# Optimization experiments

Hardware: AMD Instinct MI355X
Metric: run time of the kernel (lower is better)

Reference implementation:

```python
import jax, jax.numpy as jnp
import numpy as np

B, T, E = 2, 2048, 1024   # batch, block_size, emb_d
H, D = 16, 64             # heads, head_size


def setup_inputs() -> dict:
    key = jax.random.key(0)
    ks = jax.random.split(key, 7)
    s = 1.0 / np.sqrt(E)
    inputs = jax.random.normal(ks[0], (B, T, E), dtype=jnp.float32)
    k_w = jax.random.uniform(ks[1], (H, E, D), jnp.float32, -s, s)
    k_b = jax.random.uniform(ks[2], (H, D), jnp.float32, -s, s)
    q_w = jax.random.uniform(ks[3], (H, E, D), jnp.float32, -s, s)
    q_b = jax.random.uniform(ks[4], (H, D), jnp.float32, -s, s)
    v_w = jax.random.uniform(ks[5], (H, E, D), jnp.float32, -s, s)
    v_b = jax.random.uniform(ks[6], (H, D), jnp.float32, -s, s)
    return {"inputs": inputs, "k_w": k_w, "k_b": k_b,
            "q_w": q_w, "q_b": q_b, "v_w": v_w, "v_b": v_b}


def reference(inputs, k_w, k_b, q_w, q_b, v_w, v_b):
    # Per-head linear projections, vectorized over heads: (B,T,E)x(H,E,D)->(B,H,T,D)
    k = jnp.einsum('bte,hed->bhtd', inputs, k_w) + k_b[None, :, None, :]
    q = jnp.einsum('bte,hed->bhtd', inputs, q_w) + q_b[None, :, None, :]
    v = jnp.einsum('bte,hed->bhtd', inputs, v_w) + v_b[None, :, None, :]

    scale = D ** (-0.5)
    # scores: (B,H,Tq,Tk)
    w = jnp.einsum('bhtd,bhsd->bhts', q, k) * scale
    tril = jnp.tril(jnp.ones((T, T), dtype=bool))
    w = jnp.where(tril[None, None, :, :], w, -jnp.inf)
    # NOTE: original torch code does softmax(weights, dim=1) on a (B,T,T)
    # tensor, i.e. over the QUERY axis. Faithfully reproduce: axis=-2 here.
    w = jax.nn.softmax(w, axis=-2)
    out = jnp.einsum('bhts,bhsd->bhtd', w, v)           # (B,H,T,D)
    # concat heads along last dim, head-major order matching torch.cat
    return out.transpose(0, 2, 1, 3).reshape(B, T, H * D)
```

## Files before the change

kernel.cpp:

```cpp
#include <hip/hip_runtime.h>
#include <hip/hip_bf16.h>
#include <math.h>

#define B_ 2
#define T_ 2048
#define E_ 1024
#define H_ 16
#define D_ 64
#define NT_ 32
#define QSCALE 0.180336880f

typedef __attribute__((ext_vector_type(8))) short bf16x8;
typedef __attribute__((ext_vector_type(4))) float f32x4;

#if __has_builtin(__builtin_amdgcn_exp2f)
#define EXP2(x) __builtin_amdgcn_exp2f(x)
#else
#define EXP2(x) exp2f(x)
#endif

__device__ __forceinline__ unsigned short f2bf(float x) {
  union { float f; unsigned u; } v; v.f = x;
  unsigned r = v.u + 0x7FFFu + ((v.u >> 16) & 1u);
  return (unsigned short)(r >> 16);
}
__device__ __forceinline__ unsigned pk2bf(float a, float b) {
  __hip_bfloat162 h = __float22bfloat162_rn(make_float2(a, b));
  union { __hip_bfloat162 h; unsigned u; } c; c.h = h; return c.u;
}

__device__ __forceinline__ void dma8(const unsigned short* g, int gstride,
                                     unsigned short* l, int lane)
{
  const int r = lane >> 3, bg = (lane & 7) ^ (r & 7);
  __builtin_amdgcn_global_load_lds(
      (const __attribute__((address_space(1))) void*)(g + (size_t)r * gstride + bg * 8),
      (__attribute__((address_space(3))) void*)l, 16, 0, 0);
}
__device__ __forceinline__ bf16x8 frag(const unsigned short* tile, int row, int g) {
  return *(const bf16x8*)(tile + row * 64 + (((g ^ row) & 7) << 3));
}

__global__ __launch_bounds__(256) void inpack_kernel(const float* __restrict__ in,
                                                     unsigned short* __restrict__ o) {
  const size_t i = ((size_t)blockIdx.x * 256 + threadIdx.x) * 8;
  float4 f0 = *(const float4*)(in + i);
  float4 f1 = *(const float4*)(in + i + 4);
  unsigned u[4] = { pk2bf(f0.x, f0.y), pk2bf(f0.z, f0.w),
                    pk2bf(f1.x, f1.y), pk2bf(f1.z, f1.w) };
  *(bf16x8*)(o + i) = *(const bf16x8*)u;
}

__global__ __launch_bounds__(256) void wpack_kernel(
    const float* __restrict__ qw, const float* __restrict__ kw, const float* __restrict__ vw,
    unsigned short* __restrict__ qwt, unsigned short* __restrict__ kwt,
    unsigned short* __restrict__ vwt)
{
  __shared__ float s[64][65];
  const int tid = threadIdx.x;
  const int e0 = blockIdx.x * 64, h = blockIdx.y, z = blockIdx.z;
  const float* w = (z == 0) ? qw : (z == 1) ? kw : vw;
  unsigned short* o = (z == 0) ? qwt : (z == 1) ? kwt : vwt;
  {
    const int r = tid >> 2;
    #pragma unroll
    for (int p = 0; p < 4; ++p) {
      const int c = (tid & 3) * 4 + p * 16;
      float4 f = *(const float4*)(w + ((size_t)(h * E_ + e0 + r)) * D_ + c);
      s[r][c] = f.x; s[r][c+1] = f.y; s[r][c+2] = f.z; s[r][c+3] = f.w;
    }
  }
  __syncthreads();
  {
    const int d = tid >> 2, ec = (tid & 3) * 16;
    unsigned short tmp[16];
    #pragma unroll
    for (int j = 0; j < 16; ++j) tmp[j] = f2bf(s[ec + j][d]);
    unsigned short* dst = o + ((size_t)(h * D_ + d)) * E_ + e0 + ec;
    *(bf16x8*)(dst)     = *(const bf16x8*)&tmp[0];
    *(bf16x8*)(dst + 8) = *(const bf16x8*)&tmp[8];
  }
}

__global__ __launch_bounds__(256) void proj_kernel(
    const unsigned short* __restrict__ in16,
    const unsigned short* __restrict__ qwt, const unsigned short* __restrict__ kwt,
    const unsigned short* __restrict__ vwt,
    const float* __restrict__ qb, const float* __restrict__ kb, const float* __restrict__ vb,
    unsigned short* __restrict__ qo, unsigned short* __restrict__ ko,
    unsigned short* __restrict__ vt)
{
  __shared__ __align__(16) unsigned short in_s[2][128 * 64];
  __shared__ __align__(16) unsigned short w_s[2][3][64 * 64];
  const int tid = threadIdx.x;
  const int lane = tid & 63, wv = tid >> 6;
  const int l15 = lane & 15, quad = lane >> 4;
  const int t0 = blockIdx.x * 128, h = blockIdx.y, b = blockIdx.z;
  const int bh = b * H_ + h;
  const unsigned short* wts[3] = { qwt, kwt, vwt };

  f32x4 acc[3][2][4];
  #pragma unroll
  for (int x = 0; x < 3; ++x)
    #pragma unroll
    for (int s = 0; s < 2; ++s)
      #pragma unroll
      for (int nb = 0; nb < 4; ++nb) acc[x][s][nb] = (f32x4){0.f, 0.f, 0.f, 0.f};

#define PROJ_STAGE(e0_, bi_)                                                      \
  {                                                                               \
    const unsigned short* gin = in16 + ((size_t)(b * T_ + t0)) * E_ + (e0_);      \
    _Pragma("unroll")                                                             \
    for (int p = 0; p < 4; ++p) {                                                 \
      const int br = wv * 32 + p * 8;                                             \
      dma8(gin + (size_t)br * E_, E_, &in_s[bi_][br * 64], lane);                 \
    }                                                                             \
    _Pragma("unroll")                                                             \
    for (int j = 0; j < 6; ++j) {                                                 \
      const int idx = wv * 6 + j;                                                 \
      const int x = idx >> 3, br = (idx & 7) * 8;                                 \
      dma8(wts[x] + ((size_t)(h * D_ + br)) * E_ + (e0_), E_,                     \
           &w_s[bi_][x][br * 64], lane);                                          \
    }                                                                             \
  }

  PROJ_STAGE(0, 0);
  __syncthreads();
  for (int e = 0; e < 16; ++e) {
    const int bi = e & 1;
    if (e < 15) PROJ_STAGE((e + 1) * 64, bi ^ 1);
    const unsigned short* is = in_s[bi];
    #pragma unroll
    for (int kk = 0; kk < 2; ++kk) {
      const int g0 = kk * 4 + quad;
      bf16x8 a0 = frag(is, wv * 32 + l15, g0);
      bf16x8 a1 = frag(is, wv * 32 + 16 + l15, g0);
      #pragma unroll
      for (int x = 0; x < 3; ++x) {
        const unsigned short* ws = w_s[bi][x];
        #pragma unroll
        for (int nb = 0; nb < 4; ++nb) {
          bf16x8 bfr = frag(ws, nb * 16 + l15, g0);
          acc[x][0][nb] = __builtin_amdgcn_mfma_f32_16x16x32_bf16(a0, bfr, acc[x][0][nb], 0, 0, 0);
          acc[x][1][nb] = __builtin_amdgcn_mfma_f32_16x16x32_bf16(a1, bfr, acc[x][1][nb], 0, 0, 0);
        }
      }
    }
    __syncthreads();
  }
#undef PROJ_STAGE

  const size_t obase = (size_t)bh * T_;
  #pragma unroll
  for (int x = 0; x < 2; ++x) {
    const float scl = (x == 0) ? QSCALE : 1.0f;
    const float* bias = (x == 0) ? qb : kb;
    unsigned short* outp = (x == 0) ? qo : ko;
    #pragma unroll
    for (int nb = 0; nb < 4; ++nb) {
      const int d = nb * 16 + l15;
      const float bvv = bias[h * D_ + d];
      #pragma unroll
      for (int s = 0; s < 2; ++s)
        #pragma unroll
        for (int r = 0; r < 4; ++r) {
          const int t = t0 + wv * 32 + s * 16 + quad * 4 + r;
          outp[(obase + t) * D_ + d] = f2bf((acc[x][s][nb][r] + bvv) * scl);
        }
    }
  }
  #pragma unroll
  for (int nb = 0; nb < 4; ++nb) {
    const int d = nb * 16 + l15;
    const float bvv = vb[h * D_ + d];
    #pragma unroll
    for (int s = 0; s < 2; ++s) {
      const int t = t0 + wv * 32 + s * 16 + quad * 4;
      unsigned short pk[4];
      #pragma unroll
      for (int r = 0; r < 4; ++r) pk[r] = f2bf(acc[2][s][nb][r] + bvv);
      *(ushort4*)(vt + ((size_t)(bh * D_ + d)) * T_ + t) = *(const ushort4*)pk;
    }
  }
}

__global__ __launch_bounds__(256) void stats_kernel(
    const unsigned short* __restrict__ q, const unsigned short* __restrict__ k,
    float* __restrict__ l)
{
  __shared__ __align__(16) unsigned short q_s[2][64 * 64];
  __shared__ float red[4][64];
  const int tid = threadIdx.x;
  const int lane = tid & 63, wv = tid >> 6;
  const int l15 = lane & 15, quad = lane >> 4;
  const int sa = blockIdx.x >> 1, p = blockIdx.x & 1;
  const int tt0 = sa + ((sa ^ p) & 1);
  if (tt0 >= NT_) return;
  const int bh = blockIdx.z * H_ + blockIdx.y;
  const int s0 = sa * 64;
  const unsigned short* qbase = q + (size_t)bh * T_ * 64;

  bf16x8 kf[4][2];
  #pragma unroll
  for (int nb = 0; nb < 4; ++nb)
    #pragma unroll
    for (int kk = 0; kk < 2; ++kk)
      kf[nb][kk] = *(const bf16x8*)(k + ((size_t)(bh * T_ + s0 + nb * 16 + l15)) * 64
                                      + kk * 32 + quad * 8);

  #pragma unroll
  for (int pp = 0; pp < 2; ++pp) {
    const int br = wv * 16 + pp * 8;
    dma8(qbase + (size_t)(tt0 * 64 + br) * 64, 64, &q_s[0][br * 64], lane);
  }
  __syncthreads();

  float lsum[4] = {0.f, 0.f, 0.f, 0.f};

  for (int tt = tt0, i = 0; tt < NT_; tt += 2, ++i) {
    const int bi = i & 1;
    if (tt + 2 < NT_) {
      #pragma unroll
      for (int pp = 0; pp < 2; ++pp) {
        const int br = wv * 16 + pp * 8;
        dma8(qbase + (size_t)((tt + 2) * 64 + br) * 64, 64, &q_s[bi ^ 1][br * 64], lane);
      }
    }
    bf16x8 a0 = frag(q_s[bi], wv * 16 + l15, quad);
    bf16x8 a1 = frag(q_s[bi], wv * 16 + l15, 4 + quad);
    f32x4 sacc[4];
    #pragma unroll
    for (int nb = 0; nb < 4; ++nb) sacc[nb] = (f32x4){0.f, 0.f, 0.f, 0.f};
    #pragma unroll
    for (int nb = 0; nb < 4; ++nb) {
      sacc[nb] = __builtin_amdgcn_mfma_f32_16x16x32_bf16(a0, kf[nb][0], sacc[nb], 0, 0, 0);
      sacc[nb] = __builtin_amdgcn_mfma_f32_16x16x32_bf16(a1, kf[nb][1], sacc[nb], 0, 0, 0);
    }
    if (tt == sa) {
      const int tbase = tt * 64 + wv * 16 + quad * 4;
      #pragma unroll
      for (int nb = 0; nb < 4; ++nb) {
        const int s = s0 + nb * 16 + l15;
        #pragma unroll
        for (int r = 0; r < 4; ++r)
          lsum[nb] += (tbase + r >= s) ? EXP2(sacc[nb][r]) : 0.f;
      }
    } else {
      #pragma unroll
      for (int nb = 0; nb < 4; ++nb)
        #pragma unroll
        for (int r = 0; r < 4; ++r) lsum[nb] += EXP2(sacc[nb][r]);
    }
    __syncthreads();
  }
  #pragma unroll
  for (int nb = 0; nb < 4; ++nb) {
    lsum[nb] += __shfl_xor(lsum[nb], 16);
    lsum[nb] += __shfl_xor(lsum[nb], 32);
  }
  if (lane < 16) {
    #pragma unroll
    for (int nb = 0; nb < 4; ++nb) red[wv][nb * 16 + lane] = lsum[nb];
  }
  __syncthreads();
  if (tid < 64)
    unsafeAtomicAdd(&l[(size_t)bh * T_ + s0 + tid],
                    red[0][tid] + red[1][tid] + red[2][tid] + red[3][tid]);
}

__global__ __launch_bounds__(256) void out_kernel(
    const unsigned short* __restrict__ q, const unsigned short* __restrict__ k,
    const unsigned short* __restrict__ vt, const float* __restrict__ l,
    float* __restrict__ out)
{
  __shared__ __align__(16) unsigned short k_s[2][64 * 64];
  __shared__ __align__(16) unsigned short vt_s[2][64 * 64];
  __shared__ __align__(16) unsigned short u_s[4][16][72];
  __shared__ float rl_sh[2][64];
  const int tid = threadIdx.x;
  const int lane = tid & 63, wv = tid >> 6;
  const int l15 = lane & 15, quad = lane >> 4;
  const int jt = 31 - (blockIdx.x >> 1), p = blockIdx.x & 1;
  if (jt < p) return;
  const int n_u = (jt - p) / 2 + 1;
  const int bh = blockIdx.z * H_ + blockIdx.y;
  const int t0 = jt * 64;
  const unsigned short* kbase = k + (size_t)bh * T_ * 64;
  const unsigned short* vbase = vt + (size_t)bh * D_ * T_;
  const float* lbase = l + (size_t)bh * T_;

  const unsigned short* qrow = q + (size_t)(bh * T_ + t0 + wv * 16 + l15) * 64;
  bf16x8 qf0 = *(const bf16x8*)(qrow + quad * 8);
  bf16x8 qf1 = *(const bf16x8*)(qrow + 32 + quad * 8);

  {
    const int s0 = p * 64;
    #pragma unroll
    for (int pp = 0; pp < 2; ++pp) {
      const int br = wv * 16 + pp * 8;
      dma8(kbase + (size_t)(s0 + br) * 64, 64, &k_s[0][br * 64], lane);
      dma8(vbase + (size_t)br * T_ + s0, T_, &vt_s[0][br * 64], lane);
    }
    if (tid < 64) rl_sh[0][tid] = 1.0f / lbase[s0 + tid];
  }
  __syncthreads();

  f32x4 oacc[4];
  #pragma unroll
  for (int nb = 0; nb < 4; ++nb) oacc[nb] = (f32x4){0.f, 0.f, 0.f, 0.f};

  unsigned short* urow = &u_s[wv][l15][0];
  const int tcol = t0 + wv * 16 + l15;

  for (int i = 0; i < n_u; ++i) {
    const int st = p + 2 * i;
    const int s0 = st * 64;
    const int bi = i & 1;
    if (i + 1 < n_u) {
      const int s1 = s0 + 128;
      #pragma unroll
      for (int pp = 0; pp < 2; ++pp) {
        const int br = wv * 16 + pp * 8;
        dma8(kbase + (size_t)(s1 + br) * 64, 64, &k_s[bi ^ 1][br * 64], lane);
        dma8(vbase + (size_t)br * T_ + s1, T_, &vt_s[bi ^ 1][br * 64], lane);
      }
      if (tid < 64) rl_sh[bi ^ 1][tid] = 1.0f / lbase[s1 + tid];
    }
    const unsigned short* ks = k_s[bi];
    f32x4 sacc[4];
    #pragma unroll
    for (int mb = 0; mb < 4; ++mb) sacc[mb] = (f32x4){0.f, 0.f, 0.f, 0.f};
    #pragma unroll
    for (int mb = 0; mb < 4; ++mb) {
      bf16x8 ka0 = frag(ks, mb * 16 + l15, quad);
      bf16x8 ka1 = frag(ks, mb * 16 + l15, 4 + quad);
      sacc[mb] = __builtin_amdgcn_mfma_f32_16x16x32_bf16(ka0, qf0, sacc[mb], 0, 0, 0);
      sacc[mb] = __builtin_amdgcn_mfma_f32_16x16x32_bf16(ka1, qf1, sacc[mb], 0, 0, 0);
    }
    const float* rlb = rl_sh[bi];
    if (st == jt) {
      #pragma unroll
      for (int mb = 0; mb < 4; ++mb) {
        const int sbase = s0 + mb * 16 + quad * 4;
        float4 rv = *(const float4*)&rlb[mb * 16 + quad * 4];
        float uu[4] = { EXP2(sacc[mb][0]) * rv.x, EXP2(sacc[mb][1]) * rv.y,
                        EXP2(sacc[mb][2]) * rv.z, EXP2(sacc[mb][3]) * rv.w };
        #pragma unroll
        for (int r = 0; r < 4; ++r) if (tcol < sbase + r) uu[r] = 0.f;
        *(uint2*)(urow + mb * 16 + quad * 4) =
            make_uint2(pk2bf(uu[0], uu[1]), pk2bf(uu[2], uu[3]));
      }
    } else {
      #pragma unroll
      for (int mb = 0; mb < 4; ++mb) {
        float4 rv = *(const float4*)&rlb[mb * 16 + quad * 4];
        float uu[4] = { EXP2(sacc[mb][0]) * rv.x, EXP2(sacc[mb][1]) * rv.y,
                        EXP2(sacc[mb][2]) * rv.z, EXP2(sacc[mb][3]) * rv.w };
        *(uint2*)(urow + mb * 16 + quad * 4) =
            make_uint2(pk2bf(uu[0], uu[1]), pk2bf(uu[2], uu[3]));
      }
    }
    const unsigned short* vs = vt_s[bi];
    #pragma unroll
    for (int kk = 0; kk < 2; ++kk) {
      bf16x8 ua = *(const bf16x8*)(urow + kk * 32 + quad * 8);
      #pragma unroll
      for (int nb = 0; nb < 4; ++nb)
        oacc[nb] = __builtin_amdgcn_mfma_f32_16x16x32_bf16(
            ua, frag(vs, nb * 16 + l15, kk * 4 + quad), oacc[nb], 0, 0, 0);
    }
    __syncthreads();
  }
  #pragma unroll
  for (int nb = 0; nb < 4; ++nb) {
    const int d = nb * 16 + l15;
    #pragma unroll
    for (int r = 0; r < 4; ++r) {
      const int t = t0 + wv * 16 + quad * 4 + r;
      unsafeAtomicAdd(&out[((size_t)(blockIdx.z * T_ + t)) * (H_ * D_) + blockIdx.y * D_ + d],
                      oacc[nb][r]);
    }
  }
}

extern "C" void kernel_launch(void* const* d_in, const int* in_sizes, int n_in,
                              void* d_out, int out_size, void* d_ws, size_t ws_size,
                              hipStream_t stream) {
  const float* in = (const float*)d_in[0];
  const float* kw = (const float*)d_in[1];
  const float* kb = (const float*)d_in[2];
  const float* qw = (const float*)d_in[3];
  const float* qb = (const float*)d_in[4];
  const float* vw = (const float*)d_in[5];
  const float* vb = (const float*)d_in[6];
  float* out = (float*)d_out;

  unsigned short* p = (unsigned short*)d_ws;
  const size_t inz = (size_t)B_ * T_ * E_;
  const size_t wz  = (size_t)H_ * D_ * E_;
  const size_t qz  = (size_t)B_ * H_ * T_ * D_;
  unsigned short* in16 = p;            p += inz;
  unsigned short* qwt  = p;            p += wz;
  unsigned short* kwt  = p;            p += wz;
  unsigned short* vwt  = p;            p += wz;
  unsigned short* q16  = p;            p += qz;
  unsigned short* k16  = p;            p += qz;
  unsigned short* vtb  = p;            p += qz;
  float* lbuf = (float*)p;

  hipMemsetAsync(lbuf, 0, (size_t)B_ * H_ * T_ * sizeof(float), stream);
  hipMemsetAsync(out, 0, (size_t)out_size * sizeof(float), stream);

  dim3 blk(256);
  inpack_kernel<<<dim3(inz / 2048), blk, 0, stream>>>(in, in16);
  wpack_kernel <<<dim3(E_ / 64, H_, 3), blk, 0, stream>>>(qw, kw, vw, qwt, kwt, vwt);
  proj_kernel  <<<dim3(T_ / 128, H_, B_), blk, 0, stream>>>(in16, qwt, kwt, vwt,
                                                            qb, kb, vb, q16, k16, vtb);
  stats_kernel <<<dim3(2 * NT_, H_, B_), blk, 0, stream>>>(q16, k16, lbuf);
  out_kernel   <<<dim3(2 * NT_, H_, B_), blk, 0, stream>>>(q16, k16, vtb, lbuf, out);
}
```

Before: 209.1 us.

## Drop split-K atomics, fold log-normalizer into score accumulators, vectorize stores

The stats and output kernels no longer split each tile's work across two blocks. One block now covers the whole causal range, so the two memsets and all float atomics go away. The stats kernel writes -log2 of each column sum, and the output kernel preloads that value into the score accumulator, which removes the reciprocal and multiply per element. The projection kernel swaps MFMA operands for q/k and the output kernel does the same for P·V, so results land in a layout that allows vectorized ushort4/float4 stores. The grid is reordered with the head index fastest and occupancy hints are added. In exchange, the output kernel loses its double buffering and now syncs twice per iteration, and the longest blocks carry twice the serial work.

```diff
diff --git a/kernel.cpp b/kernel.cpp
--- a/kernel.cpp
+++ b/kernel.cpp
@@ -141,8 +141,13 @@
         #pragma unroll
         for (int nb = 0; nb < 4; ++nb) {
           bf16x8 bfr = frag(ws, nb * 16 + l15, g0);
-          acc[x][0][nb] = __builtin_amdgcn_mfma_f32_16x16x32_bf16(a0, bfr, acc[x][0][nb], 0, 0, 0);
-          acc[x][1][nb] = __builtin_amdgcn_mfma_f32_16x16x32_bf16(a1, bfr, acc[x][1][nb], 0, 0, 0);
+          if (x < 2) {
+            acc[x][0][nb] = __builtin_amdgcn_mfma_f32_16x16x32_bf16(bfr, a0, acc[x][0][nb], 0, 0, 0);
+            acc[x][1][nb] = __builtin_amdgcn_mfma_f32_16x16x32_bf16(bfr, a1, acc[x][1][nb], 0, 0, 0);
+          } else {
+            acc[x][0][nb] = __builtin_amdgcn_mfma_f32_16x16x32_bf16(a0, bfr, acc[x][0][nb], 0, 0, 0);
+            acc[x][1][nb] = __builtin_amdgcn_mfma_f32_16x16x32_bf16(a1, bfr, acc[x][1][nb], 0, 0, 0);
+          }
         }
       }
     }
@@ -158,15 +163,16 @@
     unsigned short* outp = (x == 0) ? qo : ko;
     #pragma unroll
     for (int nb = 0; nb < 4; ++nb) {
-      const int d = nb * 16 + l15;
-      const float bvv = bias[h * D_ + d];
-      #pragma unroll
-      for (int s = 0; s < 2; ++s)
+      float bias4[4];
+      *(float4*)bias4 = *(const float4*)&bias[h * D_ + nb * 16 + quad * 4];
+      #pragma unroll
+      for (int s = 0; s < 2; ++s) {
+        const int t = t0 + wv * 32 + s * 16 + l15;
+        unsigned short pk[4];
         #pragma unroll
-        for (int r = 0; r < 4; ++r) {
-          const int t = t0 + wv * 32 + s * 16 + quad * 4 + r;
-          outp[(obase + t) * D_ + d] = f2bf((acc[x][s][nb][r] + bvv) * scl);
-        }
+        for (int r = 0; r < 4; ++r) pk[r] = f2bf((acc[x][s][nb][r] + bias4[r]) * scl);
+        *(ushort4*)(outp + (obase + t) * D_ + nb * 16 + quad * 4) = *(const ushort4*)pk;
+      }
     }
   }
   #pragma unroll
@@ -184,19 +190,17 @@
   }
 }
 
-__global__ __launch_bounds__(256) void stats_kernel(
+__global__ __launch_bounds__(256, 6) void stats_kernel(
     const unsigned short* __restrict__ q, const unsigned short* __restrict__ k,
-    float* __restrict__ l)
+    float* __restrict__ lg)
 {
   __shared__ __align__(16) unsigned short q_s[2][64 * 64];
   __shared__ float red[4][64];
   const int tid = threadIdx.x;
   const int lane = tid & 63, wv = tid >> 6;
   const int l15 = lane & 15, quad = lane >> 4;
-  const int sa = blockIdx.x >> 1, p = blockIdx.x & 1;
-  const int tt0 = sa + ((sa ^ p) & 1);
-  if (tt0 >= NT_) return;
-  const int bh = blockIdx.z * H_ + blockIdx.y;
+  const int h = blockIdx.x, b = blockIdx.y, sa = blockIdx.z;
+  const int bh = b * H_ + h;
   const int s0 = sa * 64;
   const unsigned short* qbase = q + (size_t)bh * T_ * 64;
 
@@ -211,19 +215,19 @@
   #pragma unroll
   for (int pp = 0; pp < 2; ++pp) {
     const int br = wv * 16 + pp * 8;
-    dma8(qbase + (size_t)(tt0 * 64 + br) * 64, 64, &q_s[0][br * 64], lane);
+    dma8(qbase + (size_t)(sa * 64 + br) * 64, 64, &q_s[0][br * 64], lane);
   }
   __syncthreads();
 
   float lsum[4] = {0.f, 0.f, 0.f, 0.f};
 
-  for (int tt = tt0, i = 0; tt < NT_; tt += 2, ++i) {
+  for (int tt = sa, i = 0; tt < NT_; ++tt, ++i) {
     const int bi = i & 1;
-    if (tt + 2 < NT_) {
+    if (tt + 1 < NT_) {
       #pragma unroll
       for (int pp = 0; pp < 2; ++pp) {
         const int br = wv * 16 + pp * 8;
-        dma8(qbase + (size_t)((tt + 2) * 64 + br) * 64, 64, &q_s[bi ^ 1][br * 64], lane);
+        dma8(qbase + (size_t)((tt + 1) * 64 + br) * 64, 64, &q_s[bi ^ 1][br * 64], lane);
       }
     }
     bf16x8 a0 = frag(q_s[bi], wv * 16 + l15, quad);
@@ -263,88 +267,73 @@
     for (int nb = 0; nb < 4; ++nb) red[wv][nb * 16 + lane] = lsum[nb];
   }
   __syncthreads();
-  if (tid < 64)
-    unsafeAtomicAdd(&l[(size_t)bh * T_ + s0 + tid],
-                    red[0][tid] + red[1][tid] + red[2][tid] + red[3][tid]);
-}
-
-__global__ __launch_bounds__(256) void out_kernel(
+  if (tid < 64) {
+    const float L = red[0][tid] + red[1][tid] + red[2][tid] + red[3][tid];
+    lg[(size_t)bh * T_ + s0 + tid] = -__log2f(L);
+  }
+}
+
+__global__ __launch_bounds__(256, 6) void out_kernel(
     const unsigned short* __restrict__ q, const unsigned short* __restrict__ k,
-    const unsigned short* __restrict__ vt, const float* __restrict__ l,
+    const unsigned short* __restrict__ vt, const float* __restrict__ lg,
     float* __restrict__ out)
 {
-  __shared__ __align__(16) unsigned short k_s[2][64 * 64];
-  __shared__ __align__(16) unsigned short vt_s[2][64 * 64];
+  __shared__ __align__(16) unsigned short k_s[64 * 64];
+  __shared__ __align__(16) unsigned short vt_s[64 * 64];
   __shared__ __align__(16) unsigned short u_s[4][16][72];
-  __shared__ float rl_sh[2][64];
+  __shared__ float lg_sh[64];
   const int tid = threadIdx.x;
   const int lane = tid & 63, wv = tid >> 6;
   const int l15 = lane & 15, quad = lane >> 4;
-  const int jt = 31 - (blockIdx.x >> 1), p = blockIdx.x & 1;
-  if (jt < p) return;
-  const int n_u = (jt - p) / 2 + 1;
-  const int bh = blockIdx.z * H_ + blockIdx.y;
+  const int h = blockIdx.x, b = blockIdx.y, jt = 31 - blockIdx.z;
+  const int bh = b * H_ + h;
   const int t0 = jt * 64;
   const unsigned short* kbase = k + (size_t)bh * T_ * 64;
   const unsigned short* vbase = vt + (size_t)bh * D_ * T_;
-  const float* lbase = l + (size_t)bh * T_;
+  const float* lgbase = lg + (size_t)bh * T_;
 
   const unsigned short* qrow = q + (size_t)(bh * T_ + t0 + wv * 16 + l15) * 64;
   bf16x8 qf0 = *(const bf16x8*)(qrow + quad * 8);
   bf16x8 qf1 = *(const bf16x8*)(qrow + 32 + quad * 8);
 
-  {
-    const int s0 = p * 64;
+  f32x4 oacc[4];
+  #pragma unroll
+  for (int nb = 0; nb < 4; ++nb) oacc[nb] = (f32x4){0.f, 0.f, 0.f, 0.f};
+
+  unsigned short* urow = &u_s[wv][l15][0];
+  const int tcol = t0 + wv * 16 + l15;
+
+  for (int st = 0; st <= jt; ++st) {
+    const int s0 = st * 64;
+    __syncthreads();
     #pragma unroll
     for (int pp = 0; pp < 2; ++pp) {
       const int br = wv * 16 + pp * 8;
-      dma8(kbase + (size_t)(s0 + br) * 64, 64, &k_s[0][br * 64], lane);
-      dma8(vbase + (size_t)br * T_ + s0, T_, &vt_s[0][br * 64], lane);
-    }
-    if (tid < 64) rl_sh[0][tid] = 1.0f / lbase[s0 + tid];
-  }
-  __syncthreads();
-
-  f32x4 oacc[4];
-  #pragma unroll
-  for (int nb = 0; nb < 4; ++nb) oacc[nb] = (f32x4){0.f, 0.f, 0.f, 0.f};
-
-  unsigned short* urow = &u_s[wv][l15][0];
-  const int tcol = t0 + wv * 16 + l15;
-
-  for (int i = 0; i < n_u; ++i) {
-    const int st = p + 2 * i;
-    const int s0 = st * 64;
-    const int bi = i & 1;
-    if (i + 1 < n_u) {
-      const int s1 = s0 + 128;
-      #pragma unroll
-      for (int pp = 0; pp < 2; ++pp) {
-        const int br = wv * 16 + pp * 8;
-        dma8(kbase + (size_t)(s1 + br) * 64, 64, &k_s[bi ^ 1][br * 64], lane);
-        dma8(vbase + (size_t)br * T_ + s1, T_, &vt_s[bi ^ 1][br * 64], lane);
-      }
-      if (tid < 64) rl_sh[bi ^ 1][tid] = 1.0f / lbase[s1 + tid];
-    }
-    const unsigned short* ks = k_s[bi];
+      dma8(kbase + (size_t)(s0 + br) * 64, 64, &k_s[br * 64], lane);
+      dma8(vbase + (size_t)br * T_ + s0, T_, &vt_s[br * 64], lane);
+    }
+    if (tid < 64) lg_sh[tid] = lgbase[s0 + tid];
+    __syncthreads();
     f32x4 sacc[4];
     #pragma unroll
-    for (int mb = 0; mb < 4; ++mb) sacc[mb] = (f32x4){0.f, 0.f, 0.f, 0.f};
-    #pragma unroll
     for (int mb = 0; mb < 4; ++mb) {
-      bf16x8 ka0 = frag(ks, mb * 16 + l15, quad);
-      bf16x8 ka1 = frag(ks, mb * 16 + l15, 4 + quad);
+      float lg4[4];
+      *(float4*)lg4 = *(const float4*)&lg_sh[mb * 16 + quad * 4];
+      sacc[mb] = (f32x4){lg4[0], lg4[1], lg4[2], lg4[3]};
+    }
+    #pragma unroll
+    for (int mb = 0; mb < 4; ++mb) {
+      bf16x8 ka0 = frag(k_s, mb * 16 + l15, quad);
+      bf16x8 ka1 = frag(k_s, mb * 16 + l15, 4 + quad);
       sacc[mb] = __builtin_amdgcn_mfma_f32_16x16x32_bf16(ka0, qf0, sacc[mb], 0, 0, 0);
       sacc[mb] = __builtin_amdgcn_mfma_f32_16x16x32_bf16(ka1, qf1, sacc[mb], 0, 0, 0);
     }
-    const float* rlb = rl_sh[bi];
     if (st == jt) {
       #pragma unroll
       for (int mb = 0; mb < 4; ++mb) {
         const int sbase = s0 + mb * 16 + quad * 4;
-        float4 rv = *(const float4*)&rlb[mb * 16 + quad * 4];
-        float uu[4] = { EXP2(sacc[mb][0]) * rv.x, EXP2(sacc[mb][1]) * rv.y,
-                        EXP2(sacc[mb][2]) * rv.z, EXP2(sacc[mb][3]) * rv.w };
+        float uu[4] = { EXP2(sacc[mb][0]), EXP2(sacc[mb][1]),
+                        EXP2(sacc[mb][2]), EXP2(sacc[mb][3]) };
         #pragma unroll
         for (int r = 0; r < 4; ++r) if (tcol < sbase + r) uu[r] = 0.f;
         *(uint2*)(urow + mb * 16 + quad * 4) =
@@ -353,33 +342,26 @@
     } else {
       #pragma unroll
       for (int mb = 0; mb < 4; ++mb) {
-        float4 rv = *(const float4*)&rlb[mb * 16 + quad * 4];
-        float uu[4] = { EXP2(sacc[mb][0]) * rv.x, EXP2(sacc[mb][1]) * rv.y,
-                        EXP2(sacc[mb][2]) * rv.z, EXP2(sacc[mb][3]) * rv.w };
+        float uu[4] = { EXP2(sacc[mb][0]), EXP2(sacc[mb][1]),
+                        EXP2(sacc[mb][2]), EXP2(sacc[mb][3]) };
         *(uint2*)(urow + mb * 16 + quad * 4) =
             make_uint2(pk2bf(uu[0], uu[1]), pk2bf(uu[2], uu[3]));
       }
     }
-    const unsigned short* vs = vt_s[bi];
     #pragma unroll
     for (int kk = 0; kk < 2; ++kk) {
       bf16x8 ua = *(const bf16x8*)(urow + kk * 32 + quad * 8);
       #pragma unroll
       for (int nb = 0; nb < 4; ++nb)
         oacc[nb] = __builtin_amdgcn_mfma_f32_16x16x32_bf16(
-            ua, frag(vs, nb * 16 + l15, kk * 4 + quad), oacc[nb], 0, 0, 0);
-    }
-    __syncthreads();
-  }
+            frag(vt_s, nb * 16 + l15, kk * 4 + quad), ua, oacc[nb], 0, 0, 0);
+    }
+  }
+  float* orow = out + ((size_t)(b * T_ + t0 + wv * 16 + l15)) * (H_ * D_) + h * D_;
   #pragma unroll
   for (int nb = 0; nb < 4; ++nb) {
-    const int d = nb * 16 + l15;
-    #pragma unroll
-    for (int r = 0; r < 4; ++r) {
-      const int t = t0 + wv * 16 + quad * 4 + r;
-      unsafeAtomicAdd(&out[((size_t)(blockIdx.z * T_ + t)) * (H_ * D_) + blockIdx.y * D_ + d],
-                      oacc[nb][r]);
-    }
+    float o4[4] = { oacc[nb][0], oacc[nb][1], oacc[nb][2], oacc[nb][3] };
+    *(float4*)(orow + nb * 16 + quad * 4) = *(const float4*)o4;
   }
 }
 
@@ -406,16 +388,13 @@
   unsigned short* q16  = p;            p += qz;
   unsigned short* k16  = p;            p += qz;
   unsigned short* vtb  = p;            p += qz;
-  float* lbuf = (float*)p;
-
-  hipMemsetAsync(lbuf, 0, (size_t)B_ * H_ * T_ * sizeof(float), stream);
-  hipMemsetAsync(out, 0, (size_t)out_size * sizeof(float), stream);
+  float* lgbuf = (float*)p;
 
   dim3 blk(256);
   inpack_kernel<<<dim3(inz / 2048), blk, 0, stream>>>(in, in16);
   wpack_kernel <<<dim3(E_ / 64, H_, 3), blk, 0, stream>>>(qw, kw, vw, qwt, kwt, vwt);
   proj_kernel  <<<dim3(T_ / 128, H_, B_), blk, 0, stream>>>(in16, qwt, kwt, vwt,
                                                             qb, kb, vb, q16, k16, vtb);
-  stats_kernel <<<dim3(2 * NT_, H_, B_), blk, 0, stream>>>(q16, k16, lbuf);
-  out_kernel   <<<dim3(2 * NT_, H_, B_), blk, 0, stream>>>(q16, k16, vtb, lbuf, out);
-}
+  stats_kernel <<<dim3(H_, B_, NT_), blk, 0, stream>>>(q16, k16, lgbuf);
+  out_kernel   <<<dim3(H_, B_, NT_), blk, 0, stream>>>(q16, k16, vtb, lgbuf, out);
+}
```

Measured after the change: 180.2 us. -13.8%, faster.
